# Optimization experiments

Measured on AMD Instinct MI355X. Metric: run time of the kernel, lower is better.

The kernel has to match this reference:

```python
import jax, jax.numpy as jnp
import numpy as np

N0, N1, N2 = 200000, 50000, 10000   # source nodes, hop-1 targets, final targets
D, C, DEG = 256, 40, 10


def _sage(x_src, x_tgt, row, col, n_tgt, Wl, Wr, b, reduce):
    # PyG SAGEConv: lin_l(aggr(messages)) + lin_r(x_target); bias on lin_l only
    msg = x_src[row]                                   # [E, D] gather
    if reduce == 'mean':
        s = jax.ops.segment_sum(msg, col, num_segments=n_tgt)
        cnt = jax.ops.segment_sum(jnp.ones((row.shape[0], 1), msg.dtype), col, num_segments=n_tgt)
        agg = s / jnp.maximum(cnt, 1.0)
    else:
        agg = jax.ops.segment_max(msg, col, num_segments=n_tgt)
    return agg @ Wl + b + x_tgt @ Wr


def setup_inputs() -> dict:
    key = jax.random.key(0)
    ks = jax.random.split(key, 16)
    x = jax.random.normal(ks[0], (N0, D), jnp.float32)
    # every target gets exactly DEG sampled neighbors (NeighborSampler-style)
    row0 = jax.random.randint(ks[1], (N1 * DEG,), 0, N0, jnp.int32)
    col0 = jnp.repeat(jnp.arange(N1, dtype=jnp.int32), DEG)
    edge_index0 = jnp.stack([row0, col0])
    row1 = jax.random.randint(ks[2], (N2 * DEG,), 0, N1, jnp.int32)
    col1 = jnp.repeat(jnp.arange(N2, dtype=jnp.int32), DEG)
    edge_index1 = jnp.stack([row1, col1])
    s = 1.0 / np.sqrt(D)
    w = lambda k, shp: jax.random.uniform(k, shp, jnp.float32, -s, s)
    return {
        'x': x, 'edge_index0': edge_index0, 'edge_index1': edge_index1,
        'Wl_m0': w(ks[3], (D, D)), 'Wr_m0': w(ks[4], (D, D)), 'b_m0': jnp.zeros((D,), jnp.float32),
        'Wl_x0': w(ks[5], (D, D)), 'Wr_x0': w(ks[6], (D, D)), 'b_x0': jnp.zeros((D,), jnp.float32),
        'Wl_m1': w(ks[7], (D, D)), 'Wr_m1': w(ks[8], (D, D)), 'b_m1': jnp.zeros((D,), jnp.float32),
        'Wl_x1': w(ks[9], (D, D)), 'Wr_x1': w(ks[10], (D, D)), 'b_x1': jnp.zeros((D,), jnp.float32),
        'W_post': w(ks[11], (2 * D, C)), 'b_post': jnp.zeros((C,), jnp.float32),
    }


def reference(x, edge_index0, edge_index1,
              Wl_m0, Wr_m0, b_m0, Wl_x0, Wr_x0, b_x0,
              Wl_m1, Wr_m1, b_m1, Wl_x1, Wr_x1, b_x1,
              W_post, b_post):
    row0, col0 = edge_index0[0], edge_index0[1]
    row1, col1 = edge_index1[0], edge_index1[1]
    tgt0 = x[:N1]
    h_m = jax.nn.relu(_sage(x, tgt0, row0, col0, N1, Wl_m0, Wr_m0, b_m0, 'mean'))
    h_x = jax.nn.relu(_sage(x, tgt0, row0, col0, N1, Wl_x0, Wr_x0, b_x0, 'max'))
    # NOTE: faithful to source bug: layer-1 target features are the RAW x[:size[1]]
    tgt1 = x[:N2]
    o_m = _sage(h_m, tgt1, row1, col1, N2, Wl_m1, Wr_m1, b_m1, 'mean')
    o_x = _sage(h_x, tgt1, row1, col1, N2, Wl_x1, Wr_x1, b_x1, 'max')
    out = jnp.concatenate([o_m, o_x], axis=-1) @ W_post + b_post
    return jax.nn.log_softmax(out, axis=-1)
```

## Files before the change

kernel.cpp:

```cpp
#include <hip/hip_runtime.h>
#include <hip/hip_bf16.h>
#include <math.h>

#define N0v 200000
#define N1v 50000
#define N2v 10000
#define Dv  256
#define Cv  40
#define DEGv 10

typedef __attribute__((ext_vector_type(8))) short          s16x8;
typedef __attribute__((ext_vector_type(8))) unsigned short u16x8;
typedef __attribute__((ext_vector_type(4))) float          f32x4;

static __device__ __forceinline__ unsigned short f2bf(float f) {
    __hip_bfloat16 h = __float2bfloat16(f);
    return *reinterpret_cast<unsigned short*>(&h);
}
static __device__ __forceinline__ float bf2f(unsigned short u) {
    __hip_bfloat16 h = *reinterpret_cast<__hip_bfloat16*>(&u);
    return __bfloat162float(h);
}

static __device__ __forceinline__ void gload16(const void* g, void* l) {
    __builtin_amdgcn_global_load_lds(
        (const __attribute__((address_space(1))) unsigned int*)g,
        (__attribute__((address_space(3))) unsigned int*)l, 16, 0, 0);
}

__global__ __launch_bounds__(256) void conv_prep_kernel(
    const float* __restrict__ x, unsigned short* __restrict__ xb,
    const float* __restrict__ Wl0, const float* __restrict__ Wr0,
    const float* __restrict__ Wl1, const float* __restrict__ Wr1,
    const float* __restrict__ Wl2, const float* __restrict__ Wr2,
    const float* __restrict__ Wl3, const float* __restrict__ Wr3,
    unsigned short* __restrict__ WT0, unsigned short* __restrict__ WT1,
    unsigned short* __restrict__ WT2, unsigned short* __restrict__ WT3)
{
    const int b = blockIdx.x;
    const int tid = threadIdx.x;
    if (b < 25000) {
        const size_t i = ((size_t)b * 256 + tid) * 8;
        float4 v0 = *(const float4*)(x + i);
        float4 v1 = *(const float4*)(x + i + 4);
        unsigned short o[8] = { f2bf(v0.x), f2bf(v0.y), f2bf(v0.z), f2bf(v0.w),
                                f2bf(v1.x), f2bf(v1.y), f2bf(v1.z), f2bf(v1.w) };
        *(u16x8*)(xb + i) = *(u16x8*)o;
    } else {
        const int idx = b - 25000;
        const int p = idx >> 8;
        const int n = idx & 255;
        const float* Wl = (p == 0) ? Wl0 : (p == 1) ? Wl1 : (p == 2) ? Wl2 : Wl3;
        const float* Wr = (p == 0) ? Wr0 : (p == 1) ? Wr1 : (p == 2) ? Wr2 : Wr3;
        unsigned short* WT = (p == 0) ? WT0 : (p == 1) ? WT1 : (p == 2) ? WT2 : WT3;
        WT[(size_t)n * 512 + tid]       = f2bf(Wl[(size_t)tid * Dv + n]);
        WT[(size_t)n * 512 + 256 + tid] = f2bf(Wr[(size_t)tid * Dv + n]);
    }
}

__global__ __launch_bounds__(256) void agg0_kernel(
    const unsigned short* __restrict__ xb, const int* __restrict__ row,
    unsigned short* __restrict__ om, unsigned short* __restrict__ ox)
{
    const int t = blockIdx.x * 8 + (threadIdx.x >> 5);
    const int c = threadIdx.x & 31;
    const int eb = t * DEGv;
    float s[8] = {};
    float mx[8] = { -INFINITY, -INFINITY, -INFINITY, -INFINITY,
                    -INFINITY, -INFINITY, -INFINITY, -INFINITY };
#pragma unroll
    for (int k = 0; k < DEGv; ++k) {
        const int r = row[eb + k];
        u16x8 v = ((const u16x8*)xb)[(size_t)r * 32 + c];
#pragma unroll
        for (int j = 0; j < 8; ++j) {
            const float f = bf2f(v[j]);
            s[j] += f;
            mx[j] = fmaxf(mx[j], f);
        }
    }
    const float inv = 1.0f / DEGv;
    unsigned short osum[8], omax[8];
#pragma unroll
    for (int j = 0; j < 8; ++j) { osum[j] = f2bf(s[j] * inv); omax[j] = f2bf(mx[j]); }
    *(u16x8*)&om[(size_t)t * Dv + c * 8] = *(u16x8*)osum;
    *(u16x8*)&ox[(size_t)t * Dv + c * 8] = *(u16x8*)omax;
}

__global__ __launch_bounds__(256) void agg1_kernel(
    const unsigned short* __restrict__ hm, const unsigned short* __restrict__ hx,
    const int* __restrict__ row,
    unsigned short* __restrict__ om, unsigned short* __restrict__ ox)
{
    const int t = blockIdx.x * 8 + (threadIdx.x >> 5);
    const int c = threadIdx.x & 31;
    const int eb = t * DEGv;
    float s[8] = {};
    float mx[8] = { -INFINITY, -INFINITY, -INFINITY, -INFINITY,
                    -INFINITY, -INFINITY, -INFINITY, -INFINITY };
#pragma unroll
    for (int k = 0; k < DEGv; ++k) {
        const int r = row[eb + k];
        u16x8 vm = ((const u16x8*)hm)[(size_t)r * 32 + c];
        u16x8 vx = ((const u16x8*)hx)[(size_t)r * 32 + c];
#pragma unroll
        for (int j = 0; j < 8; ++j) {
            s[j]  += bf2f(vm[j]);
            mx[j]  = fmaxf(mx[j], bf2f(vx[j]));
        }
    }
    const float inv = 1.0f / DEGv;
    unsigned short osum[8], omax[8];
#pragma unroll
    for (int j = 0; j < 8; ++j) { osum[j] = f2bf(s[j] * inv); omax[j] = f2bf(mx[j]); }
    *(u16x8*)&om[(size_t)t * Dv + c * 8] = *(u16x8*)osum;
    *(u16x8*)&ox[(size_t)t * Dv + c * 8] = *(u16x8*)omax;
}

template<int RELU, int OUTBF>
__global__ __launch_bounds__(256) void gemm_mfma_kernel(
    const unsigned short* __restrict__ A1a, const unsigned short* __restrict__ A1b,
    const unsigned short* __restrict__ A2,
    const unsigned short* __restrict__ WTa, const unsigned short* __restrict__ WTb,
    const float* __restrict__ biasa, const float* __restrict__ biasb,
    void* outa, void* outb, int M, int ldc, int col_step)
{
    __shared__ unsigned short Asb[128 * 64];
    __shared__ unsigned short Bsb[256 * 64];

    const int z = blockIdx.z;
    const unsigned short* A1 = z ? A1b : A1a;
    const unsigned short* WT = z ? WTb : WTa;
    const float* bias = z ? biasb : biasa;
    void* outp = z ? outb : outa;
    const int col_off = z * col_step;

    const int tid  = threadIdx.x;
    const int lane = tid & 63;
    const int w    = tid >> 6;
    const int wrow = w >> 1;
    const int wcol = w & 1;
    const int m0   = blockIdx.x * 128;

    const int lrow = lane >> 3;
    const int scol = ((lane & 7) ^ lrow) * 8;

    const unsigned short* pA1[4];
    const unsigned short* pA2[4];
    unsigned short* lA[4];
#pragma unroll
    for (int c = 0; c < 4; ++c) {
        const int r = w * 32 + c * 8 + lrow;
        int gm = m0 + r; if (gm >= M) gm = M - 1;
        pA1[c] = A1 + (size_t)gm * Dv + scol;
        pA2[c] = A2 + (size_t)gm * Dv + scol;
        lA[c] = &Asb[(w * 32 + c * 8) * 64];
    }
    const unsigned short* pB[8];
    unsigned short* lB[8];
#pragma unroll
    for (int c = 0; c < 8; ++c) {
        const int r = w * 64 + c * 8 + lrow;
        pB[c] = WT + (size_t)r * 512 + scol;
        lB[c] = &Bsb[(w * 64 + c * 8) * 64];
    }

    const int fr = lane & 15;
    const int f7 = lane & 7;

    f32x4 acc[4][8] = {};

    for (int k0 = 0; k0 < 512; k0 += 64) {
        __syncthreads();
        if (k0 < 256) {
#pragma unroll
            for (int c = 0; c < 4; ++c) gload16(pA1[c] + k0, lA[c]);
        } else {
#pragma unroll
            for (int c = 0; c < 4; ++c) gload16(pA2[c] + (k0 - 256), lA[c]);
        }
#pragma unroll
        for (int c = 0; c < 8; ++c) gload16(pB[c] + k0, lB[c]);
        __syncthreads();

#pragma unroll
        for (int kk = 0; kk < 2; ++kk) {
            const int sl = kk * 4 + (lane >> 4);
            const int so = ((sl ^ f7) << 3);
            s16x8 af[4];
#pragma unroll
            for (int i = 0; i < 4; ++i)
                af[i] = *(const s16x8*)&Asb[(wrow * 64 + i * 16 + fr) * 64 + so];
#pragma unroll
            for (int j = 0; j < 8; ++j) {
                s16x8 bv = *(const s16x8*)&Bsb[(wcol * 128 + j * 16 + fr) * 64 + so];
#pragma unroll
                for (int i = 0; i < 4; ++i)
                    acc[i][j] = __builtin_amdgcn_mfma_f32_16x16x32_bf16(af[i], bv, acc[i][j], 0, 0, 0);
            }
        }
    }

#pragma unroll
    for (int i = 0; i < 4; ++i) {
#pragma unroll
        for (int reg = 0; reg < 4; ++reg) {
            const int gr = m0 + wrow * 64 + i * 16 + (lane >> 4) * 4 + reg;
            if (gr < M) {
#pragma unroll
                for (int j = 0; j < 8; ++j) {
                    const int gc = wcol * 128 + j * 16 + fr;
                    float v = acc[i][j][reg] + bias[gc];
                    if (RELU) v = fmaxf(v, 0.0f);
                    if (OUTBF)
                        ((unsigned short*)outp)[(size_t)gr * ldc + col_off + gc] = f2bf(v);
                    else
                        ((float*)outp)[(size_t)gr * ldc + col_off + gc] = v;
                }
            }
        }
    }
}

__global__ __launch_bounds__(256) void post_kernel(
    const unsigned short* __restrict__ ocat, const float* __restrict__ Wp,
    const float* __restrict__ bp, float* __restrict__ out, int nrows)
{
    __shared__ float sW[512 * 40];
    __shared__ float sP[7][32][40];
    __shared__ float sb[Cv];

    const int tid = threadIdx.x;

    for (int i = tid; i < 5120; i += 256)
        ((float4*)sW)[i] = ((const float4*)Wp)[i];
    if (tid < Cv) sb[tid] = bp[tid];
    __syncthreads();

    const int q = tid >> 5;
    const int r = tid & 31;
    const int t = blockIdx.x * 32 + r;
    const bool valid = (t < nrows);

    float acc[Cv] = {};
    if (valid) {
        const unsigned short* prow = ocat + (size_t)t * 512 + q * 64;
        for (int kk = 0; kk < 64; kk += 8) {
            u16x8 v = *(const u16x8*)(prow + kk);
            const float* wbase = &sW[(q * 64 + kk) * Cv];
#pragma unroll
            for (int e = 0; e < 8; ++e) {
                const float xv = bf2f(v[e]);
                const float* wr_ = wbase + e * Cv;
#pragma unroll
                for (int c4 = 0; c4 < Cv; c4 += 4) {
                    f32x4 wv = *(const f32x4*)(wr_ + c4);
                    acc[c4 + 0] += xv * wv[0];
                    acc[c4 + 1] += xv * wv[1];
                    acc[c4 + 2] += xv * wv[2];
                    acc[c4 + 3] += xv * wv[3];
                }
            }
        }
    }

    if (q > 0) {
#pragma unroll
        for (int c4 = 0; c4 < Cv; c4 += 4)
            *(f32x4*)&sP[q - 1][r][c4] = *(f32x4*)&acc[c4];
    }
    __syncthreads();

    if (q == 0 && valid) {
#pragma unroll
        for (int p = 0; p < 7; ++p)
#pragma unroll
            for (int c4 = 0; c4 < Cv; c4 += 4) {
                f32x4 pv = *(const f32x4*)&sP[p][r][c4];
                acc[c4 + 0] += pv[0];
                acc[c4 + 1] += pv[1];
                acc[c4 + 2] += pv[2];
                acc[c4 + 3] += pv[3];
            }
        float m = -INFINITY;
#pragma unroll
        for (int c = 0; c < Cv; ++c) { acc[c] += sb[c]; m = fmaxf(m, acc[c]); }
        float s = 0.0f;
#pragma unroll
        for (int c = 0; c < Cv; ++c) s += expf(acc[c] - m);
        const float lse = m + logf(s);
        float* dst = out + (size_t)t * Cv;
#pragma unroll
        for (int c4 = 0; c4 < Cv; c4 += 4) {
            float o[4] = { acc[c4] - lse, acc[c4 + 1] - lse, acc[c4 + 2] - lse, acc[c4 + 3] - lse };
            *(float4*)(dst + c4) = *(float4*)o;
        }
    }
}

extern "C" void kernel_launch(void* const* d_in, const int* in_sizes, int n_in,
                              void* d_out, int out_size, void* d_ws, size_t ws_size,
                              hipStream_t stream)
{
    const float* x      = (const float*)d_in[0];
    const int*   ei0    = (const int*)d_in[1];
    const int*   ei1    = (const int*)d_in[2];
    const float* Wl_m0  = (const float*)d_in[3];
    const float* Wr_m0  = (const float*)d_in[4];
    const float* b_m0   = (const float*)d_in[5];
    const float* Wl_x0  = (const float*)d_in[6];
    const float* Wr_x0  = (const float*)d_in[7];
    const float* b_x0   = (const float*)d_in[8];
    const float* Wl_m1  = (const float*)d_in[9];
    const float* Wr_m1  = (const float*)d_in[10];
    const float* b_m1   = (const float*)d_in[11];
    const float* Wl_x1  = (const float*)d_in[12];
    const float* Wr_x1  = (const float*)d_in[13];
    const float* b_x1   = (const float*)d_in[14];
    const float* W_post = (const float*)d_in[15];
    const float* b_post = (const float*)d_in[16];
    float* out = (float*)d_out;

    const int* row0 = ei0;
    const int* row1 = ei1;

    char* ws = (char*)d_ws;
    const size_t XB = (size_t)N0v * Dv * 2;
    const size_t NB = (size_t)N1v * Dv * 2;
    unsigned short* xb  = (unsigned short*)(ws);
    unsigned short* am  = (unsigned short*)(ws + XB);
    unsigned short* ax  = (unsigned short*)(ws + XB + NB);
    unsigned short* hm  = (unsigned short*)(ws + XB + 2 * NB);
    unsigned short* hx  = (unsigned short*)(ws + XB + 3 * NB);
    unsigned short* a1m = (unsigned short*)(ws + XB + 4 * NB);
    unsigned short* a1x = a1m + (size_t)N2v * Dv;
    unsigned short* ocat = (unsigned short*)(ws + XB + 4 * NB + (size_t)2 * N2v * Dv * 2);
    unsigned short* WT0m = ocat + (size_t)N2v * 2 * Dv;
    unsigned short* WT0x = WT0m + (size_t)256 * 512;
    unsigned short* WT1m = WT0x + (size_t)256 * 512;
    unsigned short* WT1x = WT1m + (size_t)256 * 512;

    const dim3 blk(256);

    conv_prep_kernel<<<25000 + 1024, blk, 0, stream>>>(
        x, xb,
        Wl_m0, Wr_m0, Wl_x0, Wr_x0, Wl_m1, Wr_m1, Wl_x1, Wr_x1,
        WT0m, WT0x, WT1m, WT1x);

    agg0_kernel<<<N1v / 8, blk, 0, stream>>>(xb, row0, am, ax);

    gemm_mfma_kernel<1, 1><<<dim3((N1v + 127) / 128, 1, 2), blk, 0, stream>>>(
        am, ax, xb, WT0m, WT0x, b_m0, b_x0, hm, hx, N1v, Dv, 0);

    agg1_kernel<<<N2v / 8, blk, 0, stream>>>(hm, hx, row1, a1m, a1x);
    gemm_mfma_kernel<0, 1><<<dim3((N2v + 127) / 128, 1, 2), blk, 0, stream>>>(
        a1m, a1x, xb, WT1m, WT1x, b_m1, b_x1, ocat, ocat, N2v, 2 * Dv, Dv);

    post_kernel<<<(N2v + 31) / 32, blk, 0, stream>>>(ocat, W_post, b_post, out, N2v);
}
```

Measured before the change: 217.0 us.

## Double-buffer GEMM LDS tiles with async prefetch and 512-thread blocks

Replaces the synchronous single-buffer GEMM with a double-buffered pipeline: the tiles for the next K-step (32 wide) are prefetched into a second LDS buffer while MFMAs run on the current one, with explicit vmcnt/lgkmcnt waits and barriers. The block grows to 512 threads (8 waves in a 2x4 layout, each owning a 64x64 output tile), and the swizzled LDS layout is rebuilt to match. The aim is to hide global-load latency and raise the number of waves in flight. The cost is more barriers per K-step and hand-tuned waitcnt logic that depends on each thread issuing exactly three loads per stage.

```diff
diff --git a/kernel.cpp b/kernel.cpp
--- a/kernel.cpp
+++ b/kernel.cpp
@@ -118,15 +118,15 @@
 }
 
 template<int RELU, int OUTBF>
-__global__ __launch_bounds__(256) void gemm_mfma_kernel(
+__global__ __launch_bounds__(512) void gemm_pipe_kernel(
     const unsigned short* __restrict__ A1a, const unsigned short* __restrict__ A1b,
     const unsigned short* __restrict__ A2,
     const unsigned short* __restrict__ WTa, const unsigned short* __restrict__ WTb,
     const float* __restrict__ biasa, const float* __restrict__ biasb,
     void* outa, void* outb, int M, int ldc, int col_step)
 {
-    __shared__ unsigned short Asb[128 * 64];
-    __shared__ unsigned short Bsb[256 * 64];
+    __shared__ unsigned short Asb[2][4096];
+    __shared__ unsigned short Bsb[2][8192];
 
     const int z = blockIdx.z;
     const unsigned short* A1 = z ? A1b : A1a;
@@ -138,78 +138,89 @@
     const int tid  = threadIdx.x;
     const int lane = tid & 63;
     const int w    = tid >> 6;
-    const int wrow = w >> 1;
-    const int wcol = w & 1;
+    const int wrow = w >> 2;
+    const int wcol = w & 3;
     const int m0   = blockIdx.x * 128;
 
-    const int lrow = lane >> 3;
-    const int scol = ((lane & 7) ^ lrow) * 8;
-
-    const unsigned short* pA1[4];
-    const unsigned short* pA2[4];
-    unsigned short* lA[4];
-#pragma unroll
-    for (int c = 0; c < 4; ++c) {
-        const int r = w * 32 + c * 8 + lrow;
-        int gm = m0 + r; if (gm >= M) gm = M - 1;
-        pA1[c] = A1 + (size_t)gm * Dv + scol;
-        pA2[c] = A2 + (size_t)gm * Dv + scol;
-        lA[c] = &Asb[(w * 32 + c * 8) * 64];
-    }
-    const unsigned short* pB[8];
-    unsigned short* lB[8];
-#pragma unroll
-    for (int c = 0; c < 8; ++c) {
-        const int r = w * 64 + c * 8 + lrow;
-        pB[c] = WT + (size_t)r * 512 + scol;
-        lB[c] = &Bsb[(w * 64 + c * 8) * 64];
-    }
-
+    const unsigned short *pA1s, *pA2s;
+    {
+        const int L = tid >> 3, s = tid & 7;
+        const int sig = s ^ (L & 7);
+        int gm = m0 + 2 * L + (sig >> 2);
+        if (gm >= M) gm = M - 1;
+        pA1s = A1 + (size_t)gm * Dv + ((sig & 3) << 3);
+        pA2s = A2 + (size_t)gm * Dv + ((sig & 3) << 3);
+    }
+    const unsigned short* pBs[2];
+#pragma unroll
+    for (int c = 0; c < 2; ++c) {
+        const int p = tid + c * 512;
+        const int L = p >> 3, s = p & 7;
+        const int sig = s ^ (L & 7);
+        pBs[c] = WT + (size_t)(2 * L + (sig >> 2)) * 512 + ((sig & 3) << 3);
+    }
+
+#define STAGE(bufv, k0v)                                                      \
+    {                                                                         \
+        if ((k0v) < 256) gload16(pA1s + (k0v), &Asb[bufv][tid * 8]);          \
+        else             gload16(pA2s + ((k0v) - 256), &Asb[bufv][tid * 8]);  \
+        gload16(pBs[0] + (k0v), &Bsb[bufv][tid * 8]);                         \
+        gload16(pBs[1] + (k0v), &Bsb[bufv][(tid + 512) * 8]);                 \
+    }
+
+    const int q  = lane >> 4;
     const int fr = lane & 15;
-    const int f7 = lane & 7;
-
-    f32x4 acc[4][8] = {};
-
-    for (int k0 = 0; k0 < 512; k0 += 64) {
-        __syncthreads();
-        if (k0 < 256) {
-#pragma unroll
-            for (int c = 0; c < 4; ++c) gload16(pA1[c] + k0, lA[c]);
-        } else {
-#pragma unroll
-            for (int c = 0; c < 4; ++c) gload16(pA2[c] + (k0 - 256), lA[c]);
-        }
-#pragma unroll
-        for (int c = 0; c < 8; ++c) gload16(pB[c] + k0, lB[c]);
-        __syncthreads();
-
-#pragma unroll
-        for (int kk = 0; kk < 2; ++kk) {
-            const int sl = kk * 4 + (lane >> 4);
-            const int so = ((sl ^ f7) << 3);
-            s16x8 af[4];
+    int aoff[4], boff[4];
+#pragma unroll
+    for (int i = 0; i < 4; ++i) {
+        const int r = wrow * 64 + i * 16 + fr;
+        const int L = r >> 1;
+        aoff[i] = L * 64 + (((((r & 1) << 2) + q) ^ (L & 7)) << 3);
+        const int n = wcol * 64 + i * 16 + fr;
+        const int Lb = n >> 1;
+        boff[i] = Lb * 64 + (((((n & 1) << 2) + q) ^ (Lb & 7)) << 3);
+    }
+
+    f32x4 acc[4][4] = {};
+
+    STAGE(0, 0);
+    asm volatile("" ::: "memory");
+    STAGE(1, 32);
+
+#pragma unroll
+    for (int t = 0; t < 16; ++t) {
+        if (t < 15) asm volatile("s_waitcnt vmcnt(3)" ::: "memory");
+        else        asm volatile("s_waitcnt vmcnt(0)" ::: "memory");
+        __builtin_amdgcn_s_barrier();
+
+        const int cur = t & 1;
+        s16x8 af[4], bfv[4];
+#pragma unroll
+        for (int i = 0; i < 4; ++i) {
+            af[i]  = *(const s16x8*)&Asb[cur][aoff[i]];
+            bfv[i] = *(const s16x8*)&Bsb[cur][boff[i]];
+        }
+#pragma unroll
+        for (int j = 0; j < 4; ++j)
 #pragma unroll
             for (int i = 0; i < 4; ++i)
-                af[i] = *(const s16x8*)&Asb[(wrow * 64 + i * 16 + fr) * 64 + so];
-#pragma unroll
-            for (int j = 0; j < 8; ++j) {
-                s16x8 bv = *(const s16x8*)&Bsb[(wcol * 128 + j * 16 + fr) * 64 + so];
-#pragma unroll
-                for (int i = 0; i < 4; ++i)
-                    acc[i][j] = __builtin_amdgcn_mfma_f32_16x16x32_bf16(af[i], bv, acc[i][j], 0, 0, 0);
-            }
-        }
-    }
+                acc[i][j] = __builtin_amdgcn_mfma_f32_16x16x32_bf16(af[i], bfv[j], acc[i][j], 0, 0, 0);
+
+        asm volatile("s_waitcnt lgkmcnt(0)" ::: "memory");
+        __builtin_amdgcn_s_barrier();
+        if (t < 14) STAGE(t & 1, (t + 2) * 32);
+    }
+#undef STAGE
 
 #pragma unroll
     for (int i = 0; i < 4; ++i) {
 #pragma unroll
         for (int reg = 0; reg < 4; ++reg) {
-            const int gr = m0 + wrow * 64 + i * 16 + (lane >> 4) * 4 + reg;
+            const int gr = m0 + wrow * 64 + i * 16 + q * 4 + reg;
             if (gr < M) {
 #pragma unroll
-                for (int j = 0; j < 8; ++j) {
-                    const int gc = wcol * 128 + j * 16 + fr;
+                for (int j = 0; j < 4; ++j) {
+                    const int gc = wcol * 64 + j * 16 + fr;
                     float v = acc[i][j][reg] + bias[gc];
                     if (RELU) v = fmaxf(v, 0.0f);
                     if (OUTBF)
@@ -349,11 +360,11 @@
 
     agg0_kernel<<<N1v / 8, blk, 0, stream>>>(xb, row0, am, ax);
 
-    gemm_mfma_kernel<1, 1><<<dim3((N1v + 127) / 128, 1, 2), blk, 0, stream>>>(
+    gemm_pipe_kernel<1, 1><<<dim3((N1v + 127) / 128, 1, 2), dim3(512), 0, stream>>>(
         am, ax, xb, WT0m, WT0x, b_m0, b_x0, hm, hx, N1v, Dv, 0);
 
     agg1_kernel<<<N2v / 8, blk, 0, stream>>>(hm, hx, row1, a1m, a1x);
-    gemm_mfma_kernel<0, 1><<<dim3((N2v + 127) / 128, 1, 2), blk, 0, stream>>>(
+    gemm_pipe_kernel<0, 1><<<dim3((N2v + 127) / 128, 1, 2), dim3(512), 0, stream>>>(
         a1m, a1x, xb, WT1m, WT1x, b_m1, b_x1, ocat, ocat, N2v, 2 * Dv, Dv);
 
     post_kernel<<<(N2v + 31) / 32, blk, 0, stream>>>(ocat, W_post, b_post, out, N2v);
```

New measurement: 215.5 us (median of 2 runs). No clear change (-0.7%).
